# Kernel optimization log

Hardware: AMD Instinct MI355X
Metric: run time of the kernel (lower is better)

## Reference

```python
import jax, jax.numpy as jnp
import numpy as np

N_HEAD = 16
LN_EPS = 1e-5
NEG = -10000.0


def layer_norm(x, g, b):
    mu = jnp.mean(x, axis=-1, keepdims=True)
    var = jnp.mean((x - mu) ** 2, axis=-1, keepdims=True)
    return (x - mu) * jax.lax.rsqrt(var + LN_EPS) * g + b


def split_heads(t):
    B, S, D = t.shape
    return t.reshape(B, S, N_HEAD, D // N_HEAD).transpose(0, 2, 1, 3)  # [B,H,S,hd]


def merge_heads(t):
    B, H, S, hd = t.shape
    return t.transpose(0, 2, 1, 3).reshape(B, S, H * hd)


def attn_core(q, k, v, causal):
    hd = v.shape[-1]
    w = jnp.einsum('bhqd,bhkd->bhqk', q, k) / jnp.sqrt(jnp.float32(hd)).astype(q.dtype)
    if causal:
        S = w.shape[-1]
        mask = jnp.tril(jnp.ones((S, S), dtype=bool))
        w = jnp.where(mask[None, None], w, jnp.asarray(NEG, w.dtype))
    w = jax.nn.softmax(w, axis=-1)
    return jnp.einsum('bhqk,bhkd->bhqd', w, v)


def setup_inputs() -> dict:
    key = jax.random.key(0)
    ks = jax.random.split(key, 12)
    B, S, D = 4, 1024, 1024
    sd = 0.02
    inp = {
        'x': jax.random.normal(ks[0], (B, S, D), jnp.float32),
        'ctx': jax.random.normal(ks[1], (B, S, D), jnp.float32),
        'c_attn_w': jax.random.normal(ks[2], (D, 3 * D), jnp.float32) * sd,
        'c_attn_b': jnp.zeros((3 * D,), jnp.float32),
        'self_proj_w': jax.random.normal(ks[3], (D, D), jnp.float32) * sd,
        'self_proj_b': jnp.zeros((D,), jnp.float32),
        'q_w': jax.random.normal(ks[4], (D, D), jnp.float32) * sd,
        'q_b': jnp.zeros((D,), jnp.float32),
        'kv_w': jax.random.normal(ks[5], (D, 2 * D), jnp.float32) * sd,
        'kv_b': jnp.zeros((2 * D,), jnp.float32),
        'cross_proj_w': jax.random.normal(ks[6], (D, D), jnp.float32) * sd,
        'cross_proj_b': jnp.zeros((D,), jnp.float32),
        'fc_w': jax.random.normal(ks[7], (D, 4 * D), jnp.float32) * sd,
        'fc_b': jnp.zeros((4 * D,), jnp.float32),
        'mlp_proj_w': jax.random.normal(ks[8], (4 * D, D), jnp.float32) * sd,
        'mlp_proj_b': jnp.zeros((D,), jnp.float32),
        'ln1_g': jnp.ones((D,), jnp.float32), 'ln1_b': jnp.zeros((D,), jnp.float32),
        'ln2_g': jnp.ones((D,), jnp.float32), 'ln2_b': jnp.zeros((D,), jnp.float32),
        'ln3_g': jnp.ones((D,), jnp.float32), 'ln3_b': jnp.zeros((D,), jnp.float32),
    }
    return inp


def reference(x, ctx, c_attn_w, c_attn_b, self_proj_w, self_proj_b,
              q_w, q_b, kv_w, kv_b, cross_proj_w, cross_proj_b,
              fc_w, fc_b, mlp_proj_w, mlp_proj_b,
              ln1_g, ln1_b, ln2_g, ln2_b, ln3_g, ln3_b):
    D = x.shape[-1]
    # --- causal self-attention (post-LN residual) ---
    qkv = x @ c_attn_w + c_attn_b
    q, k, v = jnp.split(qkv, 3, axis=-1)
    a = attn_core(split_heads(q), split_heads(k), split_heads(v), causal=True)
    a = merge_heads(a) @ self_proj_w + self_proj_b
    x = layer_norm(x + a, ln1_g, ln1_b)
    # --- cross-attention ---
    q = x @ q_w + q_b
    kv = ctx @ kv_w + kv_b
    k, v = jnp.split(kv, 2, axis=-1)
    a = attn_core(split_heads(q), split_heads(k), split_heads(v), causal=False)
    a = merge_heads(a) @ cross_proj_w + cross_proj_b
    x = layer_norm(x + a, ln2_g, ln2_b)
    # --- MLP (GPT2 gelu_new == tanh-approx gelu) ---
    h = jax.nn.gelu(x @ fc_w + fc_b, approximate=True)
    m = h @ mlp_proj_w + mlp_proj_b
    x = layer_norm(x + m, ln3_g, ln3_b)
    return x
```

## Files before the change

### kernel.cpp

```cpp
#include <hip/hip_runtime.h>

typedef unsigned short u16;
typedef unsigned int   u32;
typedef short bf16x8 __attribute__((ext_vector_type(8)));
typedef unsigned short u16x8 __attribute__((ext_vector_type(8)));
typedef float f32x4 __attribute__((ext_vector_type(4)));

__device__ __forceinline__ float bf2f(u16 u) {
    u32 x = ((u32)u) << 16;
    return __builtin_bit_cast(float, x);
}
__device__ __forceinline__ u16 f2bf(float f) {
    u32 u = __builtin_bit_cast(u32, f);
    u += 0x7fffu + ((u >> 16) & 1u);
    return (u16)(u >> 16);
}
__device__ __forceinline__ float gelu_f(float x) {
    const float u = 0.7978845608028654f * (x + 0.044715f * x * x * x);
    const float e = __expf(-2.f * fabsf(u));
    const float t = __builtin_copysignf((1.f - e) / (1.f + e), u);
    return 0.5f * x * (1.f + t);
}
__device__ __forceinline__ void glds16(const u16* g, u16* l) {
    __builtin_amdgcn_global_load_lds((const __attribute__((address_space(1))) u32*)g,
                                     (__attribute__((address_space(3))) u32*)l, 16, 0, 0);
}

__global__ void sniff_kernel(const u32* __restrict__ p, int* __restrict__ flag) {
    const int i = threadIdx.x;
    const u32 w = p[i * 8191 + 5];
    const u32 e = (w >> 7) & 0xFF;
    const bool absurd = (e >= 1 && e <= 90) || (e >= 160 && e <= 254);
    const unsigned long long m = __ballot(absurd);
    if (i == 0) *flag = (__popcll(m) >= 8) ? 1 : 0;
}

struct CvtPack {
    const void* src[15];
    u16*        dst[15];
    int         n[15];
};
__global__ __launch_bounds__(256) void cvt_many(CvtPack pp, const int* __restrict__ flag) {
    const int f = *flag;
    const int j = blockIdx.y;
    const void* src = pp.src[j];
    u16* dst = pp.dst[j];
    const int n = pp.n[j];
    const int idx = blockIdx.x * 256 + threadIdx.x;
    const int stride = gridDim.x * 256;
    if (f) {
        const float* s = (const float*)src;
        for (int i = idx; i < n; i += stride) dst[i] = f2bf(s[i]);
    } else {
        const u16* s = (const u16*)src;
        for (int i = idx; i < n; i += stride) dst[i] = s[i];
    }
}

__global__ __launch_bounds__(256) void transpose_cv(const void* __restrict__ src,
                                                    u16* __restrict__ dst,
                                                    int Kd, int Nd,
                                                    const int* __restrict__ flag) {
    const int f = *flag;
    __shared__ u16 t[32][33];
    const int tx = threadIdx.x & 31, ty = threadIdx.x >> 5;
    const int x  = blockIdx.x * 32 + tx;
    const int y0 = blockIdx.y * 32;
#pragma unroll
    for (int j = 0; j < 4; ++j) {
        const long idx = (long)(y0 + ty + j * 8) * Nd + x;
        t[ty + j * 8][tx] = f ? f2bf(((const float*)src)[idx]) : ((const u16*)src)[idx];
    }
    __syncthreads();
    const int xo = blockIdx.y * 32 + tx;
#pragma unroll
    for (int j = 0; j < 4; ++j)
        dst[(long)(blockIdx.x * 32 + ty + j * 8) * Kd + xo] = t[tx][ty + j * 8];
}

__global__ __launch_bounds__(256) void ln_kernel(u16* __restrict__ x,
                                                 const u16* __restrict__ g,
                                                 const u16* __restrict__ bta) {
    const int tid = threadIdx.x;
    u16* p = x + (long)blockIdx.x * 1024;
    float v[4];
    float s = 0.f, s2 = 0.f;
#pragma unroll
    for (int i = 0; i < 4; ++i) {
        v[i] = bf2f(p[tid + i * 256]);
        s += v[i]; s2 += v[i] * v[i];
    }
#pragma unroll
    for (int off = 32; off; off >>= 1) {
        s  += __shfl_xor(s, off, 64);
        s2 += __shfl_xor(s2, off, 64);
    }
    __shared__ float ps[8];
    if ((tid & 63) == 0) { ps[(tid >> 6) * 2] = s; ps[(tid >> 6) * 2 + 1] = s2; }
    __syncthreads();
    s  = ps[0] + ps[2] + ps[4] + ps[6];
    s2 = ps[1] + ps[3] + ps[5] + ps[7];
    const float mu  = s * (1.f / 1024.f);
    const float var = s2 * (1.f / 1024.f) - mu * mu;
    const float rs  = rsqrtf(var + 1e-5f);
#pragma unroll
    for (int i = 0; i < 4; ++i) {
        const int c = tid + i * 256;
        p[c] = f2bf((v[i] - mu) * rs * bf2f(g[c]) + bf2f(bta[c]));
    }
}

__global__ __launch_bounds__(256) void ln_out_kernel(const u16* __restrict__ xin,
                                                     const u16* __restrict__ g,
                                                     const u16* __restrict__ bta,
                                                     void* __restrict__ out,
                                                     const int* __restrict__ flag) {
    const int tid = threadIdx.x;
    const u16* p = xin + (long)blockIdx.x * 1024;
    float v[4];
    float s = 0.f, s2 = 0.f;
#pragma unroll
    for (int i = 0; i < 4; ++i) {
        v[i] = bf2f(p[tid + i * 256]);
        s += v[i]; s2 += v[i] * v[i];
    }
#pragma unroll
    for (int off = 32; off; off >>= 1) {
        s  += __shfl_xor(s, off, 64);
        s2 += __shfl_xor(s2, off, 64);
    }
    __shared__ float ps[8];
    if ((tid & 63) == 0) { ps[(tid >> 6) * 2] = s; ps[(tid >> 6) * 2 + 1] = s2; }
    __syncthreads();
    s  = ps[0] + ps[2] + ps[4] + ps[6];
    s2 = ps[1] + ps[3] + ps[5] + ps[7];
    const float mu  = s * (1.f / 1024.f);
    const float var = s2 * (1.f / 1024.f) - mu * mu;
    const float rs  = rsqrtf(var + 1e-5f);
    const int f = *flag;
    if (f) {
        float* o = (float*)out + (long)blockIdx.x * 1024;
#pragma unroll
        for (int i = 0; i < 4; ++i) {
            const int c = tid + i * 256;
            o[c] = (v[i] - mu) * rs * bf2f(g[c]) + bf2f(bta[c]);
        }
    } else {
        u16* o = (u16*)out + (long)blockIdx.x * 1024;
#pragma unroll
        for (int i = 0; i < 4; ++i) {
            const int c = tid + i * 256;
            o[c] = f2bf((v[i] - mu) * rs * bf2f(g[c]) + bf2f(bta[c]));
        }
    }
}

template <int BM, int BN, int EPI>
__global__ __launch_bounds__(512, (BM + BN) <= 256 ? 4 : 2)
void gemm2(const u16* __restrict__ A, const u16* __restrict__ Bt,
           const u16* __restrict__ bias, const u16* __restrict__ res,
           u16* __restrict__ C, int N, int K) {
    constexpr int WM  = BM / 2, WN = BN / 4;
    constexpr int MT  = WM / 16, NT = WN / 16;
    constexpr int ACH = BM / 8;
    constexpr int NCH = (BM + BN) / 8;
    constexpr int CPW = NCH / 8;
    constexpr int BUF = (BM + BN) * 64;

    const int tid  = threadIdx.x;
    const int wave = tid >> 6, lane = tid & 63;
    const int quad = lane >> 4, l16 = lane & 15;
    const int wm = wave >> 2, wn = wave & 3;

    const int gx  = gridDim.x;
    const int nwg = gx * gridDim.y;
    int lin = blockIdx.y * gx + blockIdx.x;
    lin = (lin & 7) * (nwg >> 3) + (lin >> 3);
    const int bx = lin % gx, by = lin / gx;
    const long m0 = (long)by * BM;
    const int  n0 = bx * BN;

    __shared__ u16 L[2][BUF];

    f32x4 acc[MT][NT];
#pragma unroll
    for (int i = 0; i < MT; ++i)
#pragma unroll
        for (int j = 0; j < NT; ++j) acc[i][j] = (f32x4){0.f, 0.f, 0.f, 0.f};

    const int ro   = lane >> 3;
    const int swzk = ((lane & 7) ^ (ro & 7)) << 3;
    const u16* gsrc[CPW];
    u16*       ldst[CPW];
#pragma unroll
    for (int c = 0; c < CPW; ++c) {
        const int ch = wave + c * 8;
        const u16* base = (ch < ACH) ? A : Bt;
        const long grow = (ch < ACH) ? (m0 + ch * 8 + ro)
                                     : ((long)n0 + (ch - ACH) * 8 + ro);
        gsrc[c] = base + grow * K + swzk;
        ldst[c] = (u16*)&L[0][ch * 512];
    }

    auto stage = [&](int ib, int kt) {
#pragma unroll
        for (int c = 0; c < CPW; ++c)
            glds16(gsrc[c] + kt, ldst[c] + ib * BUF);
    };

    const int nk = K >> 6;
    stage(0, 0);
    for (int i = 0; i < nk; ++i) {
        const int ib = i & 1;
        __syncthreads();
        if (i + 1 < nk) stage(ib ^ 1, (i + 1) << 6);
#pragma unroll
        for (int st = 0; st < 2; ++st) {
            bf16x8 af[MT], bfv[NT];
#pragma unroll
            for (int mt = 0; mt < MT; ++mt) {
                const int rr = wm * WM + mt * 16 + l16;
                af[mt] = *(const bf16x8*)&L[ib][rr * 64 + (((st * 4 + quad) ^ (rr & 7)) << 3)];
            }
#pragma unroll
            for (int nt = 0; nt < NT; ++nt) {
                const int rr = wn * WN + nt * 16 + l16;
                bfv[nt] = *(const bf16x8*)&L[ib][BM * 64 + rr * 64 +
                                                 (((st * 4 + quad) ^ (rr & 7)) << 3)];
            }
            __builtin_amdgcn_s_setprio(1);
#pragma unroll
            for (int mt = 0; mt < MT; ++mt)
#pragma unroll
                for (int nt = 0; nt < NT; ++nt)
                    acc[mt][nt] = __builtin_amdgcn_mfma_f32_16x16x32_bf16(af[mt], bfv[nt],
                                                                          acc[mt][nt], 0, 0, 0);
            __builtin_amdgcn_s_setprio(0);
        }
    }

#pragma unroll
    for (int mt = 0; mt < MT; ++mt)
#pragma unroll
        for (int r = 0; r < 4; ++r) {
            const long row = m0 + wm * WM + mt * 16 + quad * 4 + r;
#pragma unroll
            for (int nt = 0; nt < NT; ++nt) {
                const int col = n0 + wn * WN + nt * 16 + l16;
                float v = acc[mt][nt][r] + bf2f(bias[col]);
                if constexpr (EPI == 1) v += bf2f(res[row * N + col]);
                if constexpr (EPI == 2) v = gelu_f(v);
                C[row * N + col] = f2bf(v);
            }
        }
}

#define KSTR 72
#define MASKV -3.0e4f
template <bool CAUSAL>
__global__ __launch_bounds__(512) void attn2(const u16* __restrict__ Qb,
                                             const u16* __restrict__ Kb,
                                             const u16* __restrict__ Vb,
                                             u16* __restrict__ Ob,
                                             int qstride, int kvstride, int S) {
    const int tid  = threadIdx.x;
    const int wave = tid >> 6, lane = tid & 63;
    const int quad = lane >> 4, l16 = lane & 15;
    const int h = blockIdx.y, b = blockIdx.z;
    const long tokbase = (long)b * S;
    const int QT = S >> 6;

    int qtile;
    if (CAUSAL) qtile = (wave < 4) ? blockIdx.x : (QT - 1 - blockIdx.x);
    else        qtile = blockIdx.x * 2 + (wave >> 2);
    const int qbase = qtile * 64 + (wave & 3) * 16;
    const int nkt = CAUSAL ? (QT - blockIdx.x) : QT;
    const int myn = CAUSAL ? (qtile + 1) : QT;

    __shared__ u16 K_lds[2][64 * 64];
    __shared__ u16 Vt_lds[2][64 * KSTR];
    __shared__ u16 P_lds[128 * KSTR];

    const u16* qrow = Qb + (tokbase + qbase + l16) * qstride + h * 64;
    bf16x8 qf[2];
    qf[0] = *(const bf16x8*)(qrow + quad * 8);
    qf[1] = *(const bf16x8*)(qrow + 32 + quad * 8);

    f32x4 acc[4];
#pragma unroll
    for (int i = 0; i < 4; ++i) acc[i] = (f32x4){0.f, 0.f, 0.f, 0.f};
    float mrow[4], lrow[4];
#pragma unroll
    for (int r = 0; r < 4; ++r) { mrow[r] = MASKV; lrow[r] = 0.f; }

    const int kro = lane >> 3;
    const int ksw = ((lane & 7) ^ kro) << 3;
    const u16* Kln = Kb + (tokbase + wave * 8 + kro) * kvstride + h * 64 + ksw;
    const int vd = tid & 63, vkg = tid >> 6;
    const u16* Vln = Vb + (tokbase + vkg * 8) * kvstride + h * 64 + vd;

    u16x8 vreg;
    auto loadV = [&](int kt) {
#pragma unroll
        for (int jj = 0; jj < 8; ++jj)
            vreg[jj] = Vln[((long)kt * 64 + jj) * kvstride];
    };

    loadV(0);
    glds16(Kln, &K_lds[0][wave * 512]);
    *(u16x8*)(&Vt_lds[0][vd * KSTR + vkg * 8]) = vreg;
    __syncthreads();

    for (int kt = 0; kt < nkt; ++kt) {
        const int cur = kt & 1;
        const bool haveNext = (kt + 1 < nkt);
        if (haveNext) {
            glds16(Kln + (long)(kt + 1) * 64 * kvstride, &K_lds[cur ^ 1][wave * 512]);
            loadV(kt + 1);
        }
        if (kt < myn) {
            float p[4][4];
#pragma unroll
            for (int nt = 0; nt < 4; ++nt) {
                f32x4 s = (f32x4){0.f, 0.f, 0.f, 0.f};
#pragma unroll
                for (int st = 0; st < 2; ++st) {
                    bf16x8 kf = *(const bf16x8*)(&K_lds[cur][(nt * 16 + l16) * 64 +
                                                  (((st * 4 + quad) ^ (l16 & 7)) << 3)]);
                    s = __builtin_amdgcn_mfma_f32_16x16x32_bf16(qf[st], kf, s, 0, 0, 0);
                }
#pragma unroll
                for (int r = 0; r < 4; ++r) {
                    float sv = s[r] * 0.125f;
                    if (CAUSAL) {
                        const int qg  = qbase + quad * 4 + r;
                        const int kgi = kt * 64 + nt * 16 + l16;
                        if (kgi > qg) sv = MASKV;
                    }
                    p[nt][r] = sv;
                }
            }
#pragma unroll
            for (int r = 0; r < 4; ++r) {
                float mx = fmaxf(fmaxf(p[0][r], p[1][r]), fmaxf(p[2][r], p[3][r]));
#pragma unroll
                for (int off = 1; off <= 8; off <<= 1) mx = fmaxf(mx, __shfl_xor(mx, off, 64));
                const float newm  = fmaxf(mrow[r], mx);
                const float alpha = __expf(mrow[r] - newm);
                float rs = 0.f;
#pragma unroll
                for (int nt = 0; nt < 4; ++nt) {
                    p[nt][r] = __expf(p[nt][r] - newm);
                    rs += p[nt][r];
                }
#pragma unroll
                for (int off = 1; off <= 8; off <<= 1) rs += __shfl_xor(rs, off, 64);
                lrow[r] = lrow[r] * alpha + rs;
                mrow[r] = newm;
#pragma unroll
                for (int dt = 0; dt < 4; ++dt) acc[dt][r] *= alpha;
            }
#pragma unroll
            for (int nt = 0; nt < 4; ++nt)
#pragma unroll
                for (int r = 0; r < 4; ++r)
                    P_lds[(wave * 16 + quad * 4 + r) * KSTR + nt * 16 + l16] = f2bf(p[nt][r]);
#pragma unroll
            for (int st = 0; st < 2; ++st) {
                bf16x8 pf = *(const bf16x8*)(&P_lds[(wave * 16 + l16) * KSTR + st * 32 + quad * 8]);
#pragma unroll
                for (int dt = 0; dt < 4; ++dt) {
                    bf16x8 vf = *(const bf16x8*)(&Vt_lds[cur][(dt * 16 + l16) * KSTR +
                                                              st * 32 + quad * 8]);
                    acc[dt] = __builtin_amdgcn_mfma_f32_16x16x32_bf16(pf, vf, acc[dt], 0, 0, 0);
                }
            }
        }
        if (haveNext)
            *(u16x8*)(&Vt_lds[cur ^ 1][vd * KSTR + vkg * 8]) = vreg;
        __syncthreads();
    }

#pragma unroll
    for (int r = 0; r < 4; ++r) {
        const float inv = 1.f / lrow[r];
        const long row = tokbase + qbase + quad * 4 + r;
#pragma unroll
        for (int dt = 0; dt < 4; ++dt)
            Ob[row * 1024 + h * 64 + dt * 16 + l16] = f2bf(acc[dt][r] * inv);
    }
}

extern "C" void kernel_launch(void* const* d_in, const int* in_sizes, int n_in,
                              void* d_out, int out_size, void* d_ws, size_t ws_size,
                              hipStream_t stream) {
    u16* ws = (u16*)d_ws;
    u16* Wt_attn  = ws + 0;
    u16* Wt_self  = ws + 3145728;
    u16* Wt_q     = ws + 4194304;
    u16* Wt_kv    = ws + 5242880;
    u16* Wt_cross = ws + 7340032;
    u16* Wt_fc    = ws + 8388608;
    u16* Wt_mlp   = ws + 12582912;
    u16* qkv      = ws + 16777216;
    u16* q2       = ws + 16777216;
    u16* kv2      = ws + 20971520;
    u16* x2       = ws + 16777216;
    u16* hbuf     = ws + 20971520;
    u16* abuf     = ws + 29360128;
    u16* x1       = ws + 33554432;
    u16* xb       = ws + 37748736;
    u16* y3       = ws + 37748736;
    u16* ctxb     = ws + 41943040;
    u16* P        = ws + 46137344;
    u16* cab = P;            u16* spb = P + 4096;  u16* qb  = P + 8192;
    u16* kvb = P + 12288;    u16* cpb = P + 16384; u16* fcb = P + 20480;
    u16* mpb = P + 24576;
    u16* l1g = P + 28672;  u16* l1b = P + 32768;
    u16* l2g = P + 36864;  u16* l2b = P + 40960;
    u16* l3g = P + 45056;  u16* l3b = P + 49152;
    int* flag = (int*)(ws + 46137344 + 53248);

    const dim3 tb(256);
    const dim3 tg(512);
    const int NTOK = 4096;

    sniff_kernel<<<1, 64, 0, stream>>>((const u32*)d_in[0], flag);

    CvtPack pp;
    pp.src[0] = d_in[0];  pp.dst[0] = xb;   pp.n[0] = NTOK * 1024;
    pp.src[1] = d_in[1];  pp.dst[1] = ctxb; pp.n[1] = NTOK * 1024;
    pp.src[2] = d_in[3];  pp.dst[2] = cab;  pp.n[2] = 3072;
    pp.src[3] = d_in[5];  pp.dst[3] = spb;  pp.n[3] = 1024;
    pp.src[4] = d_in[7];  pp.dst[4] = qb;   pp.n[4] = 1024;
    pp.src[5] = d_in[9];  pp.dst[5] = kvb;  pp.n[5] = 2048;
    pp.src[6] = d_in[11]; pp.dst[6] = cpb;  pp.n[6] = 1024;
    pp.src[7] = d_in[13]; pp.dst[7] = fcb;  pp.n[7] = 4096;
    pp.src[8] = d_in[15]; pp.dst[8] = mpb;  pp.n[8] = 1024;
    pp.src[9] = d_in[16]; pp.dst[9] = l1g;  pp.n[9] = 1024;
    pp.src[10] = d_in[17]; pp.dst[10] = l1b; pp.n[10] = 1024;
    pp.src[11] = d_in[18]; pp.dst[11] = l2g; pp.n[11] = 1024;
    pp.src[12] = d_in[19]; pp.dst[12] = l2b; pp.n[12] = 1024;
    pp.src[13] = d_in[20]; pp.dst[13] = l3g; pp.n[13] = 1024;
    pp.src[14] = d_in[21]; pp.dst[14] = l3b; pp.n[14] = 1024;
    cvt_many<<<dim3(256, 15), tb, 0, stream>>>(pp, flag);

    transpose_cv<<<dim3(96, 32),  tb, 0, stream>>>(d_in[2],  Wt_attn,  1024, 3072, flag);
    transpose_cv<<<dim3(32, 32),  tb, 0, stream>>>(d_in[4],  Wt_self,  1024, 1024, flag);
    transpose_cv<<<dim3(32, 32),  tb, 0, stream>>>(d_in[6],  Wt_q,     1024, 1024, flag);
    transpose_cv<<<dim3(64, 32),  tb, 0, stream>>>(d_in[8],  Wt_kv,    1024, 2048, flag);
    transpose_cv<<<dim3(32, 32),  tb, 0, stream>>>(d_in[10], Wt_cross, 1024, 1024, flag);
    transpose_cv<<<dim3(128, 32), tb, 0, stream>>>(d_in[12], Wt_fc,    1024, 4096, flag);
    transpose_cv<<<dim3(32, 128), tb, 0, stream>>>(d_in[14], Wt_mlp,   4096, 1024, flag);

    gemm2<256, 256, 0><<<dim3(12, 16), tg, 0, stream>>>(xb, Wt_attn, cab, nullptr, qkv, 3072, 1024);
    attn2<true><<<dim3(8, 16, 4), tg, 0, stream>>>(qkv, qkv + 1024, qkv + 2048, abuf,
                                                   3072, 3072, 1024);
    gemm2<128, 128, 1><<<dim3(8, 32), tg, 0, stream>>>(abuf, Wt_self, spb, xb, x1, 1024, 1024);
    ln_kernel<<<NTOK, tb, 0, stream>>>(x1, l1g, l1b);

    gemm2<128, 128, 0><<<dim3(8, 32), tg, 0, stream>>>(x1,   Wt_q,  qb,  nullptr, q2,  1024, 1024);
    gemm2<128, 256, 0><<<dim3(8, 32), tg, 0, stream>>>(ctxb, Wt_kv, kvb, nullptr, kv2, 2048, 1024);
    attn2<false><<<dim3(8, 16, 4), tg, 0, stream>>>(q2, kv2, kv2 + 1024, abuf,
                                                    1024, 2048, 1024);
    gemm2<128, 128, 1><<<dim3(8, 32), tg, 0, stream>>>(abuf, Wt_cross, cpb, x1, x2, 1024, 1024);
    ln_kernel<<<NTOK, tb, 0, stream>>>(x2, l2g, l2b);

    gemm2<256, 256, 2><<<dim3(16, 16), tg, 0, stream>>>(x2, Wt_fc, fcb, nullptr, hbuf, 4096, 1024);
    gemm2<128, 128, 1><<<dim3(8, 32), tg, 0, stream>>>(hbuf, Wt_mlp, mpb, x2, y3, 1024, 4096);
    ln_out_kernel<<<NTOK, tb, 0, stream>>>(y3, l3g, l3b, d_out, flag);
}
```

Baseline: 513.2 us.

## Streamline attention softmax: prescale Q, lazy rescale, deferred row sums

Folds the 1/sqrt(hd) scale into Q once at load, applies the causal mask only on the diagonal tile, and skips the online-softmax rescale of the accumulators unless some row max grows by more than a threshold (checked with a wave vote). Per-lane partial row sums are kept and reduced across lanes only once at the end. This cuts VALU work, exp calls and shuffles in the inner loop. The costs are an extra bf16 rounding of the scaled Q and unnormalised exponents that may reach up to e^8, which slightly changes numerics.

```diff
diff --git a/kernel.cpp b/kernel.cpp
--- a/kernel.cpp
+++ b/kernel.cpp
@@ -258,7 +258,7 @@
 #define KSTR 72
 #define MASKV -3.0e4f
 template <bool CAUSAL>
-__global__ __launch_bounds__(512) void attn2(const u16* __restrict__ Qb,
+__global__ __launch_bounds__(512) void attn3(const u16* __restrict__ Qb,
                                              const u16* __restrict__ Kb,
                                              const u16* __restrict__ Vb,
                                              u16* __restrict__ Ob,
@@ -285,13 +285,18 @@
     bf16x8 qf[2];
     qf[0] = *(const bf16x8*)(qrow + quad * 8);
     qf[1] = *(const bf16x8*)(qrow + 32 + quad * 8);
+#pragma unroll
+    for (int s8 = 0; s8 < 2; ++s8)
+#pragma unroll
+        for (int j = 0; j < 8; ++j)
+            qf[s8][j] = (short)f2bf(bf2f((u16)qf[s8][j]) * 0.125f);
 
     f32x4 acc[4];
 #pragma unroll
     for (int i = 0; i < 4; ++i) acc[i] = (f32x4){0.f, 0.f, 0.f, 0.f};
-    float mrow[4], lrow[4];
-#pragma unroll
-    for (int r = 0; r < 4; ++r) { mrow[r] = MASKV; lrow[r] = 0.f; }
+    float mrow[4], lsum[4];
+#pragma unroll
+    for (int r = 0; r < 4; ++r) { mrow[r] = MASKV; lsum[r] = 0.f; }
 
     const int kro = lane >> 3;
     const int ksw = ((lane & 7) ^ kro) << 3;
@@ -330,36 +335,47 @@
                     s = __builtin_amdgcn_mfma_f32_16x16x32_bf16(qf[st], kf, s, 0, 0, 0);
                 }
 #pragma unroll
-                for (int r = 0; r < 4; ++r) {
-                    float sv = s[r] * 0.125f;
-                    if (CAUSAL) {
+                for (int r = 0; r < 4; ++r) p[nt][r] = s[r];
+            }
+            if (CAUSAL && kt == qtile) {
+#pragma unroll
+                for (int nt = 0; nt < 4; ++nt)
+#pragma unroll
+                    for (int r = 0; r < 4; ++r) {
                         const int qg  = qbase + quad * 4 + r;
                         const int kgi = kt * 64 + nt * 16 + l16;
-                        if (kgi > qg) sv = MASKV;
+                        if (kgi > qg) p[nt][r] = MASKV;
                     }
-                    p[nt][r] = sv;
+            }
+            float mx[4];
+#pragma unroll
+            for (int r = 0; r < 4; ++r) {
+                float m3 = fmaxf(fmaxf(p[0][r], p[1][r]), fmaxf(p[2][r], p[3][r]));
+#pragma unroll
+                for (int off = 1; off <= 8; off <<= 1) m3 = fmaxf(m3, __shfl_xor(m3, off, 64));
+                mx[r] = m3;
+            }
+            bool need = false;
+#pragma unroll
+            for (int r = 0; r < 4; ++r) need |= (mx[r] > mrow[r] + 8.f);
+            if (__any(need)) {
+#pragma unroll
+                for (int r = 0; r < 4; ++r) {
+                    const float newm  = fmaxf(mrow[r], mx[r]);
+                    const float alpha = __expf(mrow[r] - newm);
+                    mrow[r] = newm;
+                    lsum[r] *= alpha;
+#pragma unroll
+                    for (int dt = 0; dt < 4; ++dt) acc[dt][r] *= alpha;
                 }
             }
 #pragma unroll
-            for (int r = 0; r < 4; ++r) {
-                float mx = fmaxf(fmaxf(p[0][r], p[1][r]), fmaxf(p[2][r], p[3][r]));
-#pragma unroll
-                for (int off = 1; off <= 8; off <<= 1) mx = fmaxf(mx, __shfl_xor(mx, off, 64));
-                const float newm  = fmaxf(mrow[r], mx);
-                const float alpha = __expf(mrow[r] - newm);
-                float rs = 0.f;
-#pragma unroll
-                for (int nt = 0; nt < 4; ++nt) {
-                    p[nt][r] = __expf(p[nt][r] - newm);
-                    rs += p[nt][r];
+            for (int nt = 0; nt < 4; ++nt)
+#pragma unroll
+                for (int r = 0; r < 4; ++r) {
+                    p[nt][r] = __expf(p[nt][r] - mrow[r]);
+                    lsum[r] += p[nt][r];
                 }
-#pragma unroll
-                for (int off = 1; off <= 8; off <<= 1) rs += __shfl_xor(rs, off, 64);
-                lrow[r] = lrow[r] * alpha + rs;
-                mrow[r] = newm;
-#pragma unroll
-                for (int dt = 0; dt < 4; ++dt) acc[dt][r] *= alpha;
-            }
 #pragma unroll
             for (int nt = 0; nt < 4; ++nt)
 #pragma unroll
@@ -383,7 +399,10 @@
 
 #pragma unroll
     for (int r = 0; r < 4; ++r) {
-        const float inv = 1.f / lrow[r];
+        float rs = lsum[r];
+#pragma unroll
+        for (int off = 1; off <= 8; off <<= 1) rs += __shfl_xor(rs, off, 64);
+        const float inv = 1.f / rs;
         const long row = tokbase + qbase + quad * 4 + r;
 #pragma unroll
         for (int dt = 0; dt < 4; ++dt)
@@ -454,14 +473,14 @@
     transpose_cv<<<dim3(32, 128), tb, 0, stream>>>(d_in[14], Wt_mlp,   4096, 1024, flag);
 
     gemm2<256, 256, 0><<<dim3(12, 16), tg, 0, stream>>>(xb, Wt_attn, cab, nullptr, qkv, 3072, 1024);
-    attn2<true><<<dim3(8, 16, 4), tg, 0, stream>>>(qkv, qkv + 1024, qkv + 2048, abuf,
+    attn3<true><<<dim3(8, 16, 4), tg, 0, stream>>>(qkv, qkv + 1024, qkv + 2048, abuf,
                                                    3072, 3072, 1024);
     gemm2<128, 128, 1><<<dim3(8, 32), tg, 0, stream>>>(abuf, Wt_self, spb, xb, x1, 1024, 1024);
     ln_kernel<<<NTOK, tb, 0, stream>>>(x1, l1g, l1b);
 
-    gemm2<128, 128, 0><<<dim3(8, 32), tg, 0, stream>>>(x1,   Wt_q,  qb,  nullptr, q2,  1024, 1024);
+    gemm2<128, 128, 0><<<dim3(8, 32),  tg, 0, stream>>>(x1,   Wt_q,  qb,  nullptr, q2,  1024, 1024);
     gemm2<128, 256, 0><<<dim3(8, 32), tg, 0, stream>>>(ctxb, Wt_kv, kvb, nullptr, kv2, 2048, 1024);
-    attn2<false><<<dim3(8, 16, 4), tg, 0, stream>>>(q2, kv2, kv2 + 1024, abuf,
+    attn3<false><<<dim3(8, 16, 4), tg, 0, stream>>>(q2, kv2, kv2 + 1024, abuf,
                                                     1024, 2048, 1024);
     gemm2<128, 128, 1><<<dim3(8, 32), tg, 0, stream>>>(abuf, Wt_cross, cpb, x1, x2, 1024, 1024);
     ln_kernel<<<NTOK, tb, 0, stream>>>(x2, l2g, l2b);
```

After: 496.1 us. 1.03x faster.
